# Optimization experiments

Measured on AMD Instinct MI355X. Metric: run time of the kernel, lower is better.

## Reference

```python
import jax, jax.numpy as jnp
import numpy as np

N_HASHES = 4
CHUNK = 144
REDUCTION = 4
RES_SCALE = 1.0
NORM_EPS = 5e-5


def conv2d(x, w, b, pad):
    y = jax.lax.conv_general_dilated(
        x, w, window_strides=(1, 1), padding=[(pad, pad), (pad, pad)],
        dimension_numbers=('NCHW', 'OIHW', 'NCHW'))
    return y + b[None, :, None, None]


def add_adjacent_buckets(x):
    # x: (N, h, n_chunks, chunk, e); concat each chunk with its circular neighbors
    back = jnp.roll(x, 1, axis=2)
    fwd = jnp.roll(x, -1, axis=2)
    return jnp.concatenate([x, back, fwd], axis=3)


def setup_inputs() -> dict:
    key = jax.random.key(0)
    ks = jax.random.split(key, 6)
    x = jax.random.normal(ks[0], (1, 32, 192, 192), jnp.float32)
    w_match = jax.random.normal(ks[1], (8, 32, 3, 3), jnp.float32) * 0.05
    b_match = jnp.zeros((8,), jnp.float32)
    w_asm = jax.random.normal(ks[2], (32, 32, 1, 1), jnp.float32) * 0.05
    b_asm = jnp.zeros((32,), jnp.float32)
    rotations = jax.random.normal(ks[3], (8, N_HASHES, 64), jnp.float32)
    return {'x': x, 'w_match': w_match, 'b_match': b_match,
            'w_asm': w_asm, 'b_asm': b_asm, 'rotations': rotations}


def reference(x, w_match, b_match, w_asm, b_asm, rotations):
    N, _, H, W = x.shape
    L = H * W
    # conv_match: 3x3 conv 32->8; conv_assembly: 1x1 conv 32->32
    x_embed = conv2d(x, w_match, b_match, 1).reshape(N, -1, L).transpose(0, 2, 1)  # (N, L, 8)
    y_embed = conv2d(x, w_asm, b_asm, 0).reshape(N, -1, L).transpose(0, 2, 1)      # (N, L, 32)
    C = x_embed.shape[-1]
    hash_buckets = min(L // CHUNK + (L // CHUNK) % 2, 128)  # = 128 here

    # --- LSH hashing (non-differentiable; rotations passed in for determinism) ---
    rotated = jnp.einsum('blf,fhi->bhli', x_embed, rotations)        # (N, h, L, hb/2)
    rotated = jnp.concatenate([rotated, -rotated], axis=-1)          # (N, h, L, hb)
    hash_codes = jnp.argmax(rotated, axis=-1)                        # (N, h, L)
    hash_codes = hash_codes + (jnp.arange(N_HASHES) * hash_buckets)[None, :, None]
    hash_codes = hash_codes.reshape(N, -1)                           # (N, h*L)

    # --- sort tokens by bucket id ---
    indices = jnp.argsort(hash_codes, axis=-1)
    undo_sort = jnp.argsort(indices, axis=-1)
    mod_indices = indices % L
    x_sorted = jnp.take_along_axis(x_embed, mod_indices[:, :, None], axis=1)  # (N, h*L, 8)
    y_sorted = jnp.take_along_axis(y_embed, mod_indices[:, :, None], axis=1)  # (N, h*L, 32)

    x_b = x_sorted.reshape(N, N_HASHES, -1, C)
    y_b = y_sorted.reshape(N, N_HASHES, -1, C * REDUCTION)
    padding = (-L) % CHUNK  # static; 0 for L=192*192
    if padding:
        x_b = jnp.concatenate([x_b, x_b[:, :, -padding:, :]], axis=2)
        y_b = jnp.concatenate([y_b, y_b[:, :, -padding:, :]], axis=2)
    x_b = x_b.reshape(N, N_HASHES, -1, CHUNK, C)
    y_b = y_b.reshape(N, N_HASHES, -1, CHUNK, C * REDUCTION)

    # --- bucketed attention with adjacent buckets ---
    nrm = jnp.linalg.norm(x_b, axis=-1, keepdims=True)
    x_match = x_b / jnp.maximum(nrm, NORM_EPS)   # F.normalize(eps=5e-5)
    x_match = add_adjacent_buckets(x_match)      # (N, h, k, 3*chunk, 8)
    y_adj = add_adjacent_buckets(y_b)            # (N, h, k, 3*chunk, 32)

    raw = jnp.einsum('bhkie,bhkje->bhkij', x_b, x_match)  # (N, h, k, 144, 432)
    bucket_score = jax.scipy.special.logsumexp(raw, axis=-1, keepdims=True)
    score = jnp.exp(raw - bucket_score)
    ret = jnp.einsum('bhkij,bhkje->bhkie', score, y_adj)  # (N, h, k, 144, 32)

    ret = ret.reshape(N, N_HASHES, -1, C * REDUCTION)
    bucket_score = bucket_score.reshape(N, N_HASHES, -1)
    if padding:
        ret = ret[:, :, :-padding, :]
        bucket_score = bucket_score[:, :, :-padding]
    ret = ret.reshape(N, -1, C * REDUCTION)
    bucket_score = bucket_score.reshape(N, -1)

    # --- unsort and combine hash rounds via softmax over logsumexp scores ---
    ret = jnp.take_along_axis(ret, undo_sort[:, :, None], axis=1)
    bucket_score = jnp.take_along_axis(bucket_score, undo_sort, axis=1)
    ret = ret.reshape(N, N_HASHES, L, C * REDUCTION)
    probs = jax.nn.softmax(bucket_score.reshape(N, N_HASHES, L, 1), axis=1)
    out = jnp.sum(ret * probs, axis=1)                     # (N, L, 32)
    out = out.transpose(0, 2, 1).reshape(N, -1, H, W) * RES_SCALE + x
    return out
```

## Files before the change

### kernel.cpp

```cpp
#include <hip/hip_runtime.h>
#include <hip/hip_bf16.h>
#include <math.h>

#define LTOT 36864
#define NH 4
#define NCHUNK 256
#define CHU 144
#define NBUCK 128
#define NSEG 144
#define HW_ 192
#define VTS 148

typedef unsigned int u32;
typedef unsigned short u16;
typedef unsigned long long u64;
typedef __attribute__((ext_vector_type(4))) short short4v;
typedef __attribute__((ext_vector_type(4))) float f32x4;

__device__ __forceinline__ u32 pkbf(float a, float b){
  union { __hip_bfloat162 h2; u32 u; } cv;
  cv.h2 = __float22bfloat162_rn(float2{a,b});
  return cv.u;
}
__device__ __forceinline__ float bflo(u32 w){ return __uint_as_float(w<<16); }
__device__ __forceinline__ float bfhi(u32 w){ return __uint_as_float(w & 0xffff0000u); }

__global__ __launch_bounds__(256) void k_conv(const float* __restrict__ x,
    const float* __restrict__ wm, const float* __restrict__ bm,
    const float* __restrict__ wa, const float* __restrict__ ba,
    float* __restrict__ xe, float* __restrict__ ye)
{
  __shared__ float xs[32*108];
  const int t = threadIdx.x;
  const int id = blockIdx.x;
  const int bx = id % 12, by = id / 12;

  for (int idx=t; idx<3456; idx+=256){
    int ci = idx/108, rem = idx-ci*108;
    int iy = rem/18,  ix = rem-iy*18;
    int yy = by*4+iy-1, xx = bx*16+ix-1;
    float v = 0.f;
    if (yy>=0 && yy<HW_ && xx>=0 && xx<HW_) v = x[ci*LTOT + yy*HW_ + xx];
    xs[idx] = v;
  }
  __syncthreads();
  const int lane = t & 63;
  const int w  = __builtin_amdgcn_readfirstlane(t>>6);
  const int co0 = 2*w;
  const int cb  = 8*w;
  const int ix = lane & 15, iy = lane >> 4;
  float a0 = bm[co0], a1 = bm[co0+1];
  float acc[8];
  #pragma unroll
  for (int co=0;co<8;co++) acc[co] = ba[cb+co];
  const float* xb  = xs + iy*18 + ix;
  const float* w0p = wm + co0*288;
  const float* w1p = w0p + 288;
  for (int ci=0; ci<32; ci++){
    const float* xp = xb + ci*108;
    float x00=xp[0],  x01=xp[1],  x02=xp[2];
    float x10=xp[18], x11=xp[19], x12=xp[20];
    float x20=xp[36], x21=xp[37], x22=xp[38];
    const float* w0 = w0p + ci*9;
    const float* w1 = w1p + ci*9;
    a0 += x00*w0[0]+x01*w0[1]+x02*w0[2]
        + x10*w0[3]+x11*w0[4]+x12*w0[5]
        + x20*w0[6]+x21*w0[7]+x22*w0[8];
    a1 += x00*w1[0]+x01*w1[1]+x02*w1[2]
        + x10*w1[3]+x11*w1[4]+x12*w1[5]
        + x20*w1[6]+x21*w1[7]+x22*w1[8];
    const float* wap = wa + cb*32 + ci;
    #pragma unroll
    for (int co=0;co<8;co++) acc[co] += x11 * wap[co*32];
  }
  const int l = (by*4+iy)*HW_ + bx*16+ix;
  *(float2*)(xe + l*8 + co0) = float2{a0,a1};
  float4* yp = (float4*)(ye + l*32 + cb);
  yp[0] = make_float4(acc[0],acc[1],acc[2],acc[3]);
  yp[1] = make_float4(acc[4],acc[5],acc[6],acc[7]);
}

__global__ __launch_bounds__(256) void k_hashrank(const float* __restrict__ xe,
    const float* __restrict__ rot, int* __restrict__ code,
    int* __restrict__ lrank, int* __restrict__ hist)
{
  const int h = blockIdx.y, seg = blockIdx.x, t = threadIdx.x;
  const int l = seg*256 + t;
  const float4* qp = (const float4*)(xe + l*8);
  float4 qa = qp[0], qb = qp[1];
  float best = -INFINITY; int bi = 0;
  float worst = INFINITY; int wi = 0;
  for (int i=0; i<64; i++){
    const float* rp = rot + h*64 + i;
    float v = qa.x*rp[0]    + qa.y*rp[256]  + qa.z*rp[512]  + qa.w*rp[768]
            + qb.x*rp[1024] + qb.y*rp[1280] + qb.z*rp[1536] + qb.w*rp[1792];
    if (v > best)  { best  = v; bi = i; }
    if (v < worst) { worst = v; wi = i; }
  }
  int c = (-worst > best) ? (64+wi) : bi;
  code[h*LTOT + l] = c;

  const int lane = t & 63, w = t >> 6;
  u64 mask = ~0ull;
  #pragma unroll
  for (int bit=0; bit<7; bit++){
    u64 bset = __ballot((c>>bit)&1);
    mask &= ((c>>bit)&1) ? bset : ~bset;
  }
  int rin = __popcll(mask & ((lane==0)?0ull:(~0ull >> (64-lane))));
  int cnt = __popcll(mask);

  __shared__ int wh[4][NBUCK];
  ((int*)wh)[t] = 0; ((int*)wh)[t+256] = 0;
  __syncthreads();
  if (rin == 0) wh[w][c] = cnt;
  __syncthreads();
  int r = rin;
  for (int ww=0; ww<w; ww++) r += wh[ww][c];
  lrank[h*LTOT + l] = r;
  if (t < NBUCK) hist[(h*NSEG+seg)*NBUCK + t] = wh[0][t]+wh[1][t]+wh[2][t]+wh[3][t];
}

__global__ __launch_bounds__(512) void k_scan(const int* __restrict__ hist,
    int* __restrict__ segoff)
{
  const int h = blockIdx.x;
  const int b = threadIdx.x & 127, g = threadIdx.x >> 7;
  int vals[36];
  int sum = 0;
  #pragma unroll
  for (int i=0;i<36;i++){
    vals[i] = hist[(h*NSEG + g*36 + i)*NBUCK + b];
    sum += vals[i];
  }
  __shared__ int ps[4][NBUCK];
  __shared__ int tot[NBUCK];
  __shared__ int scv[NBUCK];
  ps[g][b] = sum;
  __syncthreads();
  if (g == 0){
    int run = 0;
    #pragma unroll
    for (int gg=0; gg<4; gg++){ int tv = ps[gg][b]; ps[gg][b] = run; run += tv; }
    tot[b] = run;
    int v = run;
    #pragma unroll
    for (int off=1; off<64; off<<=1){
      int u = __shfl_up(v, off);
      if ((b & 63) >= off) v += u;
    }
    scv[b] = v;
  }
  __syncthreads();
  int base = scv[b] - tot[b] + ((b >= 64) ? scv[63] : 0);
  int run2 = base + ps[g][b];
  #pragma unroll
  for (int i=0;i<36;i++){
    segoff[(h*NSEG + g*36 + i)*NBUCK + b] = run2;
    run2 += vals[i];
  }
}

__global__ __launch_bounds__(256) void k_scatter(const int* __restrict__ code,
    const int* __restrict__ lrank, const int* __restrict__ segoff,
    const float* __restrict__ xe, const float* __restrict__ ye,
    int* __restrict__ rankof, u16* __restrict__ Ks, u16* __restrict__ Qs,
    u16* __restrict__ Vs)
{
  const int h = blockIdx.y, seg = blockIdx.x, t = threadIdx.x;
  const int l = seg*256 + t;
  int c = code[h*LTOT + l];
  int r = segoff[(h*NSEG+seg)*NBUCK + c] + lrank[h*LTOT + l];
  rankof[h*LTOT + l] = r;

  const float4* xr = (const float4*)(xe + l*8);
  float4 a = xr[0], b = xr[1];
  float n2 = a.x*a.x+a.y*a.y+a.z*a.z+a.w*a.w
           + b.x*b.x+b.y*b.y+b.z*b.z+b.w*b.w;
  float sc = 1.0f / fmaxf(sqrtf(n2), 5e-5f);
  uint4 kk, qq;
  kk.x = pkbf(a.x*sc,a.y*sc); kk.y = pkbf(a.z*sc,a.w*sc);
  kk.z = pkbf(b.x*sc,b.y*sc); kk.w = pkbf(b.z*sc,b.w*sc);
  qq.x = pkbf(a.x,a.y); qq.y = pkbf(a.z,a.w);
  qq.z = pkbf(b.x,b.y); qq.w = pkbf(b.z,b.w);
  *(uint4*)(Ks + (size_t)(h*LTOT + r)*8) = kk;
  *(uint4*)(Qs + (size_t)(h*LTOT + r)*8) = qq;

  const float4* yr = (const float4*)(ye + l*32);
  uint4* vp = (uint4*)(Vs + (size_t)(h*LTOT + r)*32);
  #pragma unroll
  for (int e4=0; e4<4; e4++){
    float4 v0 = yr[2*e4], v1 = yr[2*e4+1];
    uint4 w;
    w.x = pkbf(v0.x,v0.y); w.y = pkbf(v0.z,v0.w);
    w.z = pkbf(v1.x,v1.y); w.w = pkbf(v1.z,v1.w);
    vp[e4] = w;
  }
}

__global__ __launch_bounds__(320) void k_attn(const u16* __restrict__ Ks,
    const u16* __restrict__ Qs, const u16* __restrict__ Vs,
    u16* __restrict__ ret_s, float* __restrict__ bs_s)
{
  __shared__ __align__(16) u16 Klds[CHU*8];
  __shared__ __align__(16) u16 Qlds[CHU*8];
  __shared__ __align__(16) u16 VT[32*VTS];
  __shared__ float qn[CHU];

  const int t = threadIdx.x;
  const int k = blockIdx.x, h = blockIdx.y;

  uint4 kpref;
  uint4 vpa0, vpa1, vpb0, vpb1;
  const int vp_i = t - 176, vp_p = vp_i >> 1, vp_hf = vp_i & 1;

  {
    const int gkb = ((k + NCHUNK-1) & (NCHUNK-1)) * CHU;
    if (t < CHU){
      kpref = *(const uint4*)(Ks + (size_t)(h*LTOT + gkb + t)*8);
      uint4 qv = *(const uint4*)(Qs + (size_t)(h*LTOT + k*CHU + t)*8);
      *(uint4*)(Qlds + t*8) = qv;
      float f0=bflo(qv.x), f1=bfhi(qv.x), f2=bflo(qv.y), f3=bfhi(qv.y);
      float f4=bflo(qv.z), f5=bfhi(qv.z), f6=bflo(qv.w), f7=bfhi(qv.w);
      qn[t] = sqrtf(f0*f0+f1*f1+f2*f2+f3*f3+f4*f4+f5*f5+f6*f6+f7*f7)*1.01f + 1e-6f;
    } else if (t >= 176){
      const uint4* ra = (const uint4*)(Vs + (size_t)(h*LTOT + gkb + 2*vp_p)*32);
      const uint4* rb = (const uint4*)(Vs + (size_t)(h*LTOT + gkb + 2*vp_p+1)*32);
      vpa0 = ra[vp_hf*2]; vpa1 = ra[vp_hf*2+1];
      vpb0 = rb[vp_hf*2]; vpb1 = rb[vp_hf*2+1];
    }
  }
  if (t < CHU){
    *(uint4*)(Klds + t*8) = kpref;
  } else if (t >= 176){
    u32 aw[8] = {vpa0.x,vpa0.y,vpa0.z,vpa0.w,vpa1.x,vpa1.y,vpa1.z,vpa1.w};
    u32 bw[8] = {vpb0.x,vpb0.y,vpb0.z,vpb0.w,vpb1.x,vpb1.y,vpb1.z,vpb1.w};
    int ebase = vp_hf*16;
    #pragma unroll
    for (int m=0;m<8;m++){
      u32 al = aw[m]&0xffffu, ah = aw[m]>>16;
      u32 bl = bw[m]&0xffffu, bh = bw[m]>>16;
      *(u32*)&VT[(ebase+2*m  )*VTS + 2*vp_p] = al | (bl<<16);
      *(u32*)&VT[(ebase+2*m+1)*VTS + 2*vp_p] = ah | (bh<<16);
    }
  }
  __syncthreads();

  const int lane = t & 63;
  const int wv = t >> 6;
  const int q = lane & 15;
  const int quad = lane >> 4;
  const int tl0 = 2*wv, tl1 = (2*wv+1 < 9) ? 2*wv+1 : 8;

  const short4v zs = {0,0,0,0};
  short4v bq0 = zs, bq1 = zs;
  if (quad < 2){
    bq0 = *(const short4v*)(Qlds + (tl0*16+q)*8 + quad*4);
    bq1 = *(const short4v*)(Qlds + (tl1*16+q)*8 + quad*4);
  }
  const float m0 = qn[tl0*16+q], m1 = qn[tl1*16+q];

  f32x4 o00={0,0,0,0}, o01={0,0,0,0}, o10={0,0,0,0}, o11={0,0,0,0};
  float s0 = 0.f, s1 = 0.f;

  for (int r=0; r<3; r++){
    if (r < 2){
      const int gkb = ((k + NCHUNK + r) & (NCHUNK-1)) * CHU;
      if (t < CHU){
        kpref = *(const uint4*)(Ks + (size_t)(h*LTOT + gkb + t)*8);
      } else if (t >= 176){
        const uint4* ra = (const uint4*)(Vs + (size_t)(h*LTOT + gkb + 2*vp_p)*32);
        const uint4* rb = (const uint4*)(Vs + (size_t)(h*LTOT + gkb + 2*vp_p+1)*32);
        vpa0 = ra[vp_hf*2]; vpa1 = ra[vp_hf*2+1];
        vpb0 = rb[vp_hf*2]; vpb1 = rb[vp_hf*2+1];
      }
    }

    #pragma unroll 3
    for (int kt=0; kt<9; kt++){
      short4v av = zs;
      if (quad < 2) av = *(const short4v*)(Klds + (kt*16+q)*8 + quad*4);
      f32x4 zc = {0.f,0.f,0.f,0.f};
      f32x4 stA = __builtin_amdgcn_mfma_f32_16x16x16bf16_1k(av, bq0, zc, 0,0,0);
      f32x4 stB = __builtin_amdgcn_mfma_f32_16x16x16bf16_1k(av, bq1, zc, 0,0,0);

      float pA0 = __expf(stA[0]-m0), pA1 = __expf(stA[1]-m0);
      float pA2 = __expf(stA[2]-m0), pA3 = __expf(stA[3]-m0);
      float pB0 = __expf(stB[0]-m1), pB1 = __expf(stB[1]-m1);
      float pB2 = __expf(stB[2]-m1), pB3 = __expf(stB[3]-m1);
      s0 += (pA0+pA1)+(pA2+pA3);
      s1 += (pB0+pB1)+(pB2+pB3);

      union { u32 u[2]; short4v s4; } pkA, pkB;
      pkA.u[0] = pkbf(pA0,pA1); pkA.u[1] = pkbf(pA2,pA3);
      pkB.u[0] = pkbf(pB0,pB1); pkB.u[1] = pkbf(pB2,pB3);

      short4v va0 = *(const short4v*)(&VT[ q    *VTS + kt*16 + quad*4]);
      short4v va1 = *(const short4v*)(&VT[(q+16)*VTS + kt*16 + quad*4]);
      o00 = __builtin_amdgcn_mfma_f32_16x16x16bf16_1k(va0, pkA.s4, o00, 0,0,0);
      o01 = __builtin_amdgcn_mfma_f32_16x16x16bf16_1k(va1, pkA.s4, o01, 0,0,0);
      o10 = __builtin_amdgcn_mfma_f32_16x16x16bf16_1k(va0, pkB.s4, o10, 0,0,0);
      o11 = __builtin_amdgcn_mfma_f32_16x16x16bf16_1k(va1, pkB.s4, o11, 0,0,0);
    }

    if (r < 2){
      __syncthreads();
      if (t < CHU){
        *(uint4*)(Klds + t*8) = kpref;
      } else if (t >= 176){
        u32 aw[8] = {vpa0.x,vpa0.y,vpa0.z,vpa0.w,vpa1.x,vpa1.y,vpa1.z,vpa1.w};
        u32 bw[8] = {vpb0.x,vpb0.y,vpb0.z,vpb0.w,vpb1.x,vpb1.y,vpb1.z,vpb1.w};
        int ebase = vp_hf*16;
        #pragma unroll
        for (int m=0;m<8;m++){
          u32 al = aw[m]&0xffffu, ah = aw[m]>>16;
          u32 bl = bw[m]&0xffffu, bh = bw[m]>>16;
          *(u32*)&VT[(ebase+2*m  )*VTS + 2*vp_p] = al | (bl<<16);
          *(u32*)&VT[(ebase+2*m+1)*VTS + 2*vp_p] = ah | (bh<<16);
        }
      }
      __syncthreads();
    }
  }

  float st0 = s0, st1 = s1;
  st0 += __shfl_xor(st0, 16); st0 += __shfl_xor(st0, 32);
  st1 += __shfl_xor(st1, 16); st1 += __shfl_xor(st1, 32);
  float inv0 = 1.0f/st0, inv1 = 1.0f/st1;

  const int row0 = h*LTOT + k*CHU + tl0*16 + q;
  const int row1 = h*LTOT + k*CHU + tl1*16 + q;
  u16* rp0 = ret_s + (size_t)row0*32;
  u16* rp1 = ret_s + (size_t)row1*32;
  uint2 wA, wB;
  wA.x = pkbf(o00[0]*inv0, o00[1]*inv0); wA.y = pkbf(o00[2]*inv0, o00[3]*inv0);
  wB.x = pkbf(o01[0]*inv0, o01[1]*inv0); wB.y = pkbf(o01[2]*inv0, o01[3]*inv0);
  *(uint2*)&rp0[quad*4]    = wA;
  *(uint2*)&rp0[16+quad*4] = wB;
  wA.x = pkbf(o10[0]*inv1, o10[1]*inv1); wA.y = pkbf(o10[2]*inv1, o10[3]*inv1);
  wB.x = pkbf(o11[0]*inv1, o11[1]*inv1); wB.y = pkbf(o11[2]*inv1, o11[3]*inv1);
  *(uint2*)&rp1[quad*4]    = wA;
  *(uint2*)&rp1[16+quad*4] = wB;
  if (quad == 0){
    bs_s[row0] = m0 + __logf(st0);
    bs_s[row1] = m1 + __logf(st1);
  }
}

__global__ __launch_bounds__(256) void k_final(const float* __restrict__ x,
    const int* __restrict__ rankof, const u16* __restrict__ ret_s,
    const float* __restrict__ bs_s, float* __restrict__ out)
{
  const int l  = blockIdx.x*64 + (threadIdx.x & 63);
  const int eg = threadIdx.x >> 6;
  int r[NH]; float bs[NH];
  #pragma unroll
  for (int h=0;h<NH;h++) r[h] = rankof[h*LTOT + l];
  #pragma unroll
  for (int h=0;h<NH;h++) bs[h] = bs_s[h*LTOT + r[h]];
  float m = fmaxf(fmaxf(bs[0],bs[1]), fmaxf(bs[2],bs[3]));
  float p[NH]; float s = 0.f;
  #pragma unroll
  for (int h=0;h<NH;h++){ p[h] = __expf(bs[h]-m); s += p[h]; }
  float inv = 1.0f/s;
  float o[8];
  #pragma unroll
  for (int e=0;e<8;e++) o[e]=0.f;
  #pragma unroll
  for (int h=0;h<NH;h++){
    float w = p[h]*inv;
    uint4 v = *(const uint4*)(ret_s + (size_t)(h*LTOT + r[h])*32 + eg*8);
    o[0] += w*bflo(v.x); o[1] += w*bfhi(v.x);
    o[2] += w*bflo(v.y); o[3] += w*bfhi(v.y);
    o[4] += w*bflo(v.z); o[5] += w*bfhi(v.z);
    o[6] += w*bflo(v.w); o[7] += w*bfhi(v.w);
  }
  #pragma unroll
  for (int e=0;e<8;e++){
    int ge = eg*8 + e;
    out[ge*LTOT + l] = o[e] + x[ge*LTOT + l];
  }
}

extern "C" void kernel_launch(void* const* d_in, const int* in_sizes, int n_in,
                              void* d_out, int out_size, void* d_ws, size_t ws_size,
                              hipStream_t stream)
{
  const float* x   = (const float*)d_in[0];
  const float* wm  = (const float*)d_in[1];
  const float* bm  = (const float*)d_in[2];
  const float* wa  = (const float*)d_in[3];
  const float* ba  = (const float*)d_in[4];
  const float* rot = (const float*)d_in[5];
  float* out = (float*)d_out;

  char* ws = (char*)d_ws;
  size_t off = 0;
  auto alloc = [&](size_t bytes)->void*{
    void* p = ws + off;
    off = (off + bytes + 255) & ~(size_t)255;
    return p;
  };
  float* xe     = (float*)alloc((size_t)LTOT*8*4);
  float* ye     = (float*)alloc((size_t)LTOT*32*4);
  int*   code   = (int*)  alloc((size_t)NH*LTOT*4);
  int*   lrank  = (int*)  alloc((size_t)NH*LTOT*4);
  int*   hist   = (int*)  alloc((size_t)NH*NSEG*NBUCK*4);
  int*   segoff = (int*)  alloc((size_t)NH*NSEG*NBUCK*4);
  int*   rankof = (int*)  alloc((size_t)NH*LTOT*4);
  u16*   Ks     = (u16*)  alloc((size_t)NH*LTOT*8*2);
  u16*   Qs     = (u16*)  alloc((size_t)NH*LTOT*8*2);
  u16*   Vs     = (u16*)  alloc((size_t)NH*LTOT*32*2);
  u16*   ret_s  = (u16*)  alloc((size_t)NH*LTOT*32*2);
  float* bs_s   = (float*)alloc((size_t)NH*LTOT*4);

  hipLaunchKernelGGL(k_conv,     dim3(576),        dim3(256), 0, stream, x, wm, bm, wa, ba, xe, ye);
  hipLaunchKernelGGL(k_hashrank, dim3(NSEG,NH),    dim3(256), 0, stream, xe, rot, code, lrank, hist);
  hipLaunchKernelGGL(k_scan,     dim3(NH),         dim3(512), 0, stream, hist, segoff);
  hipLaunchKernelGGL(k_scatter,  dim3(NSEG,NH),    dim3(256), 0, stream, code, lrank, segoff, xe, ye, rankof, Ks, Qs, Vs);
  hipLaunchKernelGGL(k_attn,     dim3(NCHUNK,NH),  dim3(320), 0, stream, Ks, Qs, Vs, ret_s, bs_s);
  hipLaunchKernelGGL(k_final,    dim3(576),        dim3(256), 0, stream, x, rankof, ret_s, bs_s, out);
}
```

Before: 140.2 us.

## Fuse conv, hash, scan and scatter into one cooperative kernel with grid syncs

Merges the four front-end kernels (conv, hash/rank, bucket scan, scatter) into a single cooperative launch that separates the phases with grid-wide syncs. Hash codes and local ranks stay in registers, so the code and lrank buffers and their global round trips go away, and three kernel launch gaps disappear. The scan now runs on one block per hash round while the rest of the grid waits at a barrier. The launch needs all 576 blocks resident at once, and each grid.sync carries its own cost.

```diff
diff --git a/kernel.cpp b/kernel.cpp
--- a/kernel.cpp
+++ b/kernel.cpp
@@ -1,6 +1,9 @@
 #include <hip/hip_runtime.h>
+#include <hip/hip_cooperative_groups.h>
 #include <hip/hip_bf16.h>
 #include <math.h>
+
+namespace cg = cooperative_groups;
 
 #define LTOT 36864
 #define NH 4
@@ -25,176 +28,162 @@
 __device__ __forceinline__ float bflo(u32 w){ return __uint_as_float(w<<16); }
 __device__ __forceinline__ float bfhi(u32 w){ return __uint_as_float(w & 0xffff0000u); }
 
-__global__ __launch_bounds__(256) void k_conv(const float* __restrict__ x,
-    const float* __restrict__ wm, const float* __restrict__ bm,
-    const float* __restrict__ wa, const float* __restrict__ ba,
-    float* __restrict__ xe, float* __restrict__ ye)
+__global__ __launch_bounds__(256, 3) void k_front(
+    const float* __restrict__ x,  const float* __restrict__ wm,
+    const float* __restrict__ bm, const float* __restrict__ wa,
+    const float* __restrict__ ba, const float* __restrict__ rot,
+    float* __restrict__ xe, float* __restrict__ ye,
+    int* __restrict__ hist, int* __restrict__ segoff,
+    int* __restrict__ rankof, u16* __restrict__ Ks, u16* __restrict__ Qs,
+    u16* __restrict__ Vs)
 {
-  __shared__ float xs[32*108];
+  cg::grid_group grid = cg::this_grid();
+  __shared__ float xs[3456];
+  __shared__ int wh[4][NBUCK];
+  __shared__ int ps[2][NBUCK];
+  __shared__ int tot[NBUCK], scv[NBUCK];
+
   const int t = threadIdx.x;
-  const int id = blockIdx.x;
-  const int bx = id % 12, by = id / 12;
-
-  for (int idx=t; idx<3456; idx+=256){
-    int ci = idx/108, rem = idx-ci*108;
-    int iy = rem/18,  ix = rem-iy*18;
-    int yy = by*4+iy-1, xx = bx*16+ix-1;
-    float v = 0.f;
-    if (yy>=0 && yy<HW_ && xx>=0 && xx<HW_) v = x[ci*LTOT + yy*HW_ + xx];
-    xs[idx] = v;
-  }
-  __syncthreads();
-  const int lane = t & 63;
-  const int w  = __builtin_amdgcn_readfirstlane(t>>6);
-  const int co0 = 2*w;
-  const int cb  = 8*w;
-  const int ix = lane & 15, iy = lane >> 4;
-  float a0 = bm[co0], a1 = bm[co0+1];
-  float acc[8];
-  #pragma unroll
-  for (int co=0;co<8;co++) acc[co] = ba[cb+co];
-  const float* xb  = xs + iy*18 + ix;
-  const float* w0p = wm + co0*288;
-  const float* w1p = w0p + 288;
-  for (int ci=0; ci<32; ci++){
-    const float* xp = xb + ci*108;
-    float x00=xp[0],  x01=xp[1],  x02=xp[2];
-    float x10=xp[18], x11=xp[19], x12=xp[20];
-    float x20=xp[36], x21=xp[37], x22=xp[38];
-    const float* w0 = w0p + ci*9;
-    const float* w1 = w1p + ci*9;
-    a0 += x00*w0[0]+x01*w0[1]+x02*w0[2]
-        + x10*w0[3]+x11*w0[4]+x12*w0[5]
-        + x20*w0[6]+x21*w0[7]+x22*w0[8];
-    a1 += x00*w1[0]+x01*w1[1]+x02*w1[2]
-        + x10*w1[3]+x11*w1[4]+x12*w1[5]
-        + x20*w1[6]+x21*w1[7]+x22*w1[8];
-    const float* wap = wa + cb*32 + ci;
+  const int seg = blockIdx.x, h = blockIdx.y;
+  const int id = h*NSEG + seg;
+
+  {
+    const int bx = id % 12, by = id / 12;
+    for (int idx=t; idx<3456; idx+=256){
+      int ci = idx/108, rem = idx-ci*108;
+      int iy = rem/18,  ix = rem-iy*18;
+      int yy = by*4+iy-1, xx = bx*16+ix-1;
+      float v = 0.f;
+      if (yy>=0 && yy<HW_ && xx>=0 && xx<HW_) v = x[ci*LTOT + yy*HW_ + xx];
+      xs[idx] = v;
+    }
+    __syncthreads();
+    const int lane = t & 63;
+    const int w  = __builtin_amdgcn_readfirstlane(t>>6);
+    const int co0 = 2*w, cb = 8*w;
+    const int ix = lane & 15, iy = lane >> 4;
+    float a0 = bm[co0], a1 = bm[co0+1];
+    float acc[8];
     #pragma unroll
-    for (int co=0;co<8;co++) acc[co] += x11 * wap[co*32];
-  }
-  const int l = (by*4+iy)*HW_ + bx*16+ix;
-  *(float2*)(xe + l*8 + co0) = float2{a0,a1};
-  float4* yp = (float4*)(ye + l*32 + cb);
-  yp[0] = make_float4(acc[0],acc[1],acc[2],acc[3]);
-  yp[1] = make_float4(acc[4],acc[5],acc[6],acc[7]);
-}
-
-__global__ __launch_bounds__(256) void k_hashrank(const float* __restrict__ xe,
-    const float* __restrict__ rot, int* __restrict__ code,
-    int* __restrict__ lrank, int* __restrict__ hist)
-{
-  const int h = blockIdx.y, seg = blockIdx.x, t = threadIdx.x;
+    for (int co=0;co<8;co++) acc[co] = ba[cb+co];
+    const float* xb  = xs + iy*18 + ix;
+    const float* w0p = wm + co0*288;
+    const float* w1p = w0p + 288;
+    for (int ci=0; ci<32; ci++){
+      const float* xp = xb + ci*108;
+      float x00=xp[0],  x01=xp[1],  x02=xp[2];
+      float x10=xp[18], x11=xp[19], x12=xp[20];
+      float x20=xp[36], x21=xp[37], x22=xp[38];
+      const float* w0 = w0p + ci*9;
+      const float* w1 = w1p + ci*9;
+      a0 += x00*w0[0]+x01*w0[1]+x02*w0[2]
+          + x10*w0[3]+x11*w0[4]+x12*w0[5]
+          + x20*w0[6]+x21*w0[7]+x22*w0[8];
+      a1 += x00*w1[0]+x01*w1[1]+x02*w1[2]
+          + x10*w1[3]+x11*w1[4]+x12*w1[5]
+          + x20*w1[6]+x21*w1[7]+x22*w1[8];
+      const float* wap = wa + cb*32 + ci;
+      #pragma unroll
+      for (int co=0;co<8;co++) acc[co] += x11 * wap[co*32];
+    }
+    const int lc = (by*4+iy)*HW_ + bx*16+ix;
+    *(float2*)(xe + lc*8 + co0) = float2{a0,a1};
+    float4* yp = (float4*)(ye + lc*32 + cb);
+    yp[0] = make_float4(acc[0],acc[1],acc[2],acc[3]);
+    yp[1] = make_float4(acc[4],acc[5],acc[6],acc[7]);
+  }
+  grid.sync();
+
   const int l = seg*256 + t;
   const float4* qp = (const float4*)(xe + l*8);
   float4 qa = qp[0], qb = qp[1];
-  float best = -INFINITY; int bi = 0;
-  float worst = INFINITY; int wi = 0;
-  for (int i=0; i<64; i++){
-    const float* rp = rot + h*64 + i;
-    float v = qa.x*rp[0]    + qa.y*rp[256]  + qa.z*rp[512]  + qa.w*rp[768]
-            + qb.x*rp[1024] + qb.y*rp[1280] + qb.z*rp[1536] + qb.w*rp[1792];
-    if (v > best)  { best  = v; bi = i; }
-    if (v < worst) { worst = v; wi = i; }
-  }
-  int c = (-worst > best) ? (64+wi) : bi;
-  code[h*LTOT + l] = c;
-
-  const int lane = t & 63, w = t >> 6;
-  u64 mask = ~0ull;
-  #pragma unroll
-  for (int bit=0; bit<7; bit++){
-    u64 bset = __ballot((c>>bit)&1);
-    mask &= ((c>>bit)&1) ? bset : ~bset;
-  }
-  int rin = __popcll(mask & ((lane==0)?0ull:(~0ull >> (64-lane))));
-  int cnt = __popcll(mask);
-
-  __shared__ int wh[4][NBUCK];
-  ((int*)wh)[t] = 0; ((int*)wh)[t+256] = 0;
-  __syncthreads();
-  if (rin == 0) wh[w][c] = cnt;
-  __syncthreads();
-  int r = rin;
-  for (int ww=0; ww<w; ww++) r += wh[ww][c];
-  lrank[h*LTOT + l] = r;
-  if (t < NBUCK) hist[(h*NSEG+seg)*NBUCK + t] = wh[0][t]+wh[1][t]+wh[2][t]+wh[3][t];
-}
-
-__global__ __launch_bounds__(512) void k_scan(const int* __restrict__ hist,
-    int* __restrict__ segoff)
-{
-  const int h = blockIdx.x;
-  const int b = threadIdx.x & 127, g = threadIdx.x >> 7;
-  int vals[36];
-  int sum = 0;
-  #pragma unroll
-  for (int i=0;i<36;i++){
-    vals[i] = hist[(h*NSEG + g*36 + i)*NBUCK + b];
-    sum += vals[i];
-  }
-  __shared__ int ps[4][NBUCK];
-  __shared__ int tot[NBUCK];
-  __shared__ int scv[NBUCK];
-  ps[g][b] = sum;
-  __syncthreads();
-  if (g == 0){
-    int run = 0;
+  int c;
+  {
+    float best = -INFINITY; int bi = 0;
+    float worst = INFINITY; int wi = 0;
+    for (int i=0; i<64; i++){
+      const float* rp = rot + h*64 + i;
+      float v = qa.x*rp[0]    + qa.y*rp[256]  + qa.z*rp[512]  + qa.w*rp[768]
+              + qb.x*rp[1024] + qb.y*rp[1280] + qb.z*rp[1536] + qb.w*rp[1792];
+      if (v > best)  { best  = v; bi = i; }
+      if (v < worst) { worst = v; wi = i; }
+    }
+    c = (-worst > best) ? (64+wi) : bi;
+  }
+  int r_local;
+  {
+    const int lane = t & 63, w = t >> 6;
+    u64 mask = ~0ull;
     #pragma unroll
-    for (int gg=0; gg<4; gg++){ int tv = ps[gg][b]; ps[gg][b] = run; run += tv; }
-    tot[b] = run;
-    int v = run;
+    for (int bit=0; bit<7; bit++){
+      u64 bset = __ballot((c>>bit)&1);
+      mask &= ((c>>bit)&1) ? bset : ~bset;
+    }
+    int rin = __popcll(mask & ((lane==0)?0ull:(~0ull >> (64-lane))));
+    int cnt = __popcll(mask);
+    ((int*)wh)[t] = 0; ((int*)wh)[t+256] = 0;
+    __syncthreads();
+    if (rin == 0) wh[w][c] = cnt;
+    __syncthreads();
+    r_local = rin;
+    for (int ww=0; ww<w; ww++) r_local += wh[ww][c];
+    if (t < NBUCK) hist[(h*NSEG+seg)*NBUCK + t] = wh[0][t]+wh[1][t]+wh[2][t]+wh[3][t];
+  }
+  grid.sync();
+
+  if (seg == 0){
+    const int b = t & 127, g = t >> 7;
+    int sum = 0;
+    for (int i=0;i<72;i++) sum += hist[(h*NSEG + g*72 + i)*NBUCK + b];
+    ps[g][b] = sum;
+    __syncthreads();
+    if (g == 0){
+      int run = 0;
+      #pragma unroll
+      for (int gg=0; gg<2; gg++){ int tv = ps[gg][b]; ps[gg][b] = run; run += tv; }
+      tot[b] = run;
+      int v = run;
+      #pragma unroll
+      for (int off=1; off<64; off<<=1){
+        int u = __shfl_up(v, off);
+        if ((b & 63) >= off) v += u;
+      }
+      scv[b] = v;
+    }
+    __syncthreads();
+    int base = scv[b] - tot[b] + ((b >= 64) ? scv[63] : 0);
+    int run2 = base + ps[g][b];
+    for (int i=0;i<72;i++){
+      segoff[(h*NSEG + g*72 + i)*NBUCK + b] = run2;
+      run2 += hist[(h*NSEG + g*72 + i)*NBUCK + b];
+    }
+  }
+  grid.sync();
+
+  {
+    int r = segoff[(h*NSEG+seg)*NBUCK + c] + r_local;
+    rankof[h*LTOT + l] = r;
+    float n2 = qa.x*qa.x+qa.y*qa.y+qa.z*qa.z+qa.w*qa.w
+             + qb.x*qb.x+qb.y*qb.y+qb.z*qb.z+qb.w*qb.w;
+    float sc = 1.0f / fmaxf(sqrtf(n2), 5e-5f);
+    uint4 kk, qq;
+    kk.x = pkbf(qa.x*sc,qa.y*sc); kk.y = pkbf(qa.z*sc,qa.w*sc);
+    kk.z = pkbf(qb.x*sc,qb.y*sc); kk.w = pkbf(qb.z*sc,qb.w*sc);
+    qq.x = pkbf(qa.x,qa.y); qq.y = pkbf(qa.z,qa.w);
+    qq.z = pkbf(qb.x,qb.y); qq.w = pkbf(qb.z,qb.w);
+    *(uint4*)(Ks + (size_t)(h*LTOT + r)*8) = kk;
+    *(uint4*)(Qs + (size_t)(h*LTOT + r)*8) = qq;
+
+    const float4* yr = (const float4*)(ye + l*32);
+    uint4* vp = (uint4*)(Vs + (size_t)(h*LTOT + r)*32);
     #pragma unroll
-    for (int off=1; off<64; off<<=1){
-      int u = __shfl_up(v, off);
-      if ((b & 63) >= off) v += u;
-    }
-    scv[b] = v;
-  }
-  __syncthreads();
-  int base = scv[b] - tot[b] + ((b >= 64) ? scv[63] : 0);
-  int run2 = base + ps[g][b];
-  #pragma unroll
-  for (int i=0;i<36;i++){
-    segoff[(h*NSEG + g*36 + i)*NBUCK + b] = run2;
-    run2 += vals[i];
-  }
-}
-
-__global__ __launch_bounds__(256) void k_scatter(const int* __restrict__ code,
-    const int* __restrict__ lrank, const int* __restrict__ segoff,
-    const float* __restrict__ xe, const float* __restrict__ ye,
-    int* __restrict__ rankof, u16* __restrict__ Ks, u16* __restrict__ Qs,
-    u16* __restrict__ Vs)
-{
-  const int h = blockIdx.y, seg = blockIdx.x, t = threadIdx.x;
-  const int l = seg*256 + t;
-  int c = code[h*LTOT + l];
-  int r = segoff[(h*NSEG+seg)*NBUCK + c] + lrank[h*LTOT + l];
-  rankof[h*LTOT + l] = r;
-
-  const float4* xr = (const float4*)(xe + l*8);
-  float4 a = xr[0], b = xr[1];
-  float n2 = a.x*a.x+a.y*a.y+a.z*a.z+a.w*a.w
-           + b.x*b.x+b.y*b.y+b.z*b.z+b.w*b.w;
-  float sc = 1.0f / fmaxf(sqrtf(n2), 5e-5f);
-  uint4 kk, qq;
-  kk.x = pkbf(a.x*sc,a.y*sc); kk.y = pkbf(a.z*sc,a.w*sc);
-  kk.z = pkbf(b.x*sc,b.y*sc); kk.w = pkbf(b.z*sc,b.w*sc);
-  qq.x = pkbf(a.x,a.y); qq.y = pkbf(a.z,a.w);
-  qq.z = pkbf(b.x,b.y); qq.w = pkbf(b.z,b.w);
-  *(uint4*)(Ks + (size_t)(h*LTOT + r)*8) = kk;
-  *(uint4*)(Qs + (size_t)(h*LTOT + r)*8) = qq;
-
-  const float4* yr = (const float4*)(ye + l*32);
-  uint4* vp = (uint4*)(Vs + (size_t)(h*LTOT + r)*32);
-  #pragma unroll
-  for (int e4=0; e4<4; e4++){
-    float4 v0 = yr[2*e4], v1 = yr[2*e4+1];
-    uint4 w;
-    w.x = pkbf(v0.x,v0.y); w.y = pkbf(v0.z,v0.w);
-    w.z = pkbf(v1.x,v1.y); w.w = pkbf(v1.z,v1.w);
-    vp[e4] = w;
+    for (int e4=0; e4<4; e4++){
+      float4 v0 = yr[2*e4], v1 = yr[2*e4+1];
+      uint4 w;
+      w.x = pkbf(v0.x,v0.y); w.y = pkbf(v0.z,v0.w);
+      w.z = pkbf(v1.x,v1.y); w.w = pkbf(v1.z,v1.w);
+      vp[e4] = w;
+    }
   }
 }
 
@@ -403,8 +392,6 @@
   };
   float* xe     = (float*)alloc((size_t)LTOT*8*4);
   float* ye     = (float*)alloc((size_t)LTOT*32*4);
-  int*   code   = (int*)  alloc((size_t)NH*LTOT*4);
-  int*   lrank  = (int*)  alloc((size_t)NH*LTOT*4);
   int*   hist   = (int*)  alloc((size_t)NH*NSEG*NBUCK*4);
   int*   segoff = (int*)  alloc((size_t)NH*NSEG*NBUCK*4);
   int*   rankof = (int*)  alloc((size_t)NH*LTOT*4);
@@ -414,10 +401,12 @@
   u16*   ret_s  = (u16*)  alloc((size_t)NH*LTOT*32*2);
   float* bs_s   = (float*)alloc((size_t)NH*LTOT*4);
 
-  hipLaunchKernelGGL(k_conv,     dim3(576),        dim3(256), 0, stream, x, wm, bm, wa, ba, xe, ye);
-  hipLaunchKernelGGL(k_hashrank, dim3(NSEG,NH),    dim3(256), 0, stream, xe, rot, code, lrank, hist);
-  hipLaunchKernelGGL(k_scan,     dim3(NH),         dim3(512), 0, stream, hist, segoff);
-  hipLaunchKernelGGL(k_scatter,  dim3(NSEG,NH),    dim3(256), 0, stream, code, lrank, segoff, xe, ye, rankof, Ks, Qs, Vs);
-  hipLaunchKernelGGL(k_attn,     dim3(NCHUNK,NH),  dim3(320), 0, stream, Ks, Qs, Vs, ret_s, bs_s);
-  hipLaunchKernelGGL(k_final,    dim3(576),        dim3(256), 0, stream, x, rankof, ret_s, bs_s, out);
+  void* fargs[] = { (void*)&x, (void*)&wm, (void*)&bm, (void*)&wa, (void*)&ba,
+                    (void*)&rot, (void*)&xe, (void*)&ye, (void*)&hist,
+                    (void*)&segoff, (void*)&rankof, (void*)&Ks, (void*)&Qs,
+                    (void*)&Vs };
+  hipLaunchCooperativeKernel((const void*)k_front, dim3(NSEG,NH), dim3(256),
+                             fargs, 0, stream);
+  hipLaunchKernelGGL(k_attn,  dim3(NCHUNK,NH), dim3(320), 0, stream, Ks, Qs, Vs, ret_s, bs_s);
+  hipLaunchKernelGGL(k_final, dim3(576),       dim3(256), 0, stream, x, rankof, ret_s, bs_s, out);
 }
```

Measured after the change: 329.5 us. 2.35x slower.
